# Kernel optimization log

Measured on AMD Instinct MI355X. Metric: run time of the kernel, lower is better.

The kernel has to match this reference:

```python
import jax, jax.numpy as jnp
import numpy as np

W_PAD = 1  # reflection pad / stencil half-width
CLAMP_MIN = 0.071
EPS = 1e-05


def _laplacian_kernel():
    k = 2 * W_PAD + 1
    ker = -jnp.ones((1, 1, k, k, k), dtype=jnp.float32)
    ker = ker.at[0, 0, W_PAD, W_PAD, W_PAD].set(float(k * k * k - 1))
    return ker  # [O=1, I=1, 3, 3, 3]


def _boundary_weight(pred):
    # pred: [B, L, D, H, W] raw logits
    B, L, D, H, Wd = pred.shape
    ps = jax.nn.softmax(pred, axis=1).astype(jnp.float32)
    # reflect-pad spatial dims by 1, then clamp (matches torch: pad then clamp)
    p = jnp.pad(ps, ((0, 0), (0, 0), (1, 1), (1, 1), (1, 1)), mode='reflect')
    p = jnp.clip(p, CLAMP_MIN)
    # single-channel 3x3x3 stencil applied independently per (batch, label)
    x = p.reshape(B * L, 1, D + 2, H + 2, Wd + 2)
    bt = jax.lax.conv_general_dilated(
        x, _laplacian_kernel(), window_strides=(1, 1, 1), padding='VALID',
        dimension_numbers=('NCDHW', 'OIDHW', 'NCDHW'))
    bt = jnp.abs(bt).reshape(B, L, D, H, Wd)
    bt = jax.lax.stop_gradient(bt)  # torch .detach()
    return 0.5 / (bt + 0.5)


def _dice_bpm(y_pred, y_true, bpm):
    vol_axes = tuple(range(2, y_pred.ndim))  # spatial dims
    top = 2.0 * jnp.sum(y_true * y_pred * bpm, axis=vol_axes)
    bottom = jnp.clip(jnp.sum((y_true + y_pred) * bpm, axis=vol_axes), EPS)
    return -jnp.mean(top / bottom)


def setup_inputs() -> dict:
    key = jax.random.key(0)
    k1, k2 = jax.random.split(key)
    shape = (2, 8, 128, 128, 128)
    pred = jax.random.normal(k1, shape, dtype=jnp.float32)
    target = jax.random.uniform(k2, shape, dtype=jnp.float32)
    return {"pred": pred, "target": target}


def reference(pred, target):
    focal_weight = _boundary_weight(pred)
    return _dice_bpm(pred, target, focal_weight)
```

## Files before the change

kernel.cpp:

```cpp
#include <hip/hip_runtime.h>
#include <hip/hip_fp16.h>

constexpr int Dd = 128, Hh = 128, Ww = 128;
constexpr int B_ = 2, L_ = 8;
constexpr int S_SP = Dd * Hh * Ww;
constexpr float CLAMP_MIN = 0.071f;
constexpr float EPS = 1e-5f;

constexpr int DCH = 8;
constexpr int NDC = Dd / DCH;
constexpr int NHG = Hh / 16;
constexpr int BLK_PER_P = NDC * NHG;
constexpr int NBLK2 = B_ * L_ * BLK_PER_P;

__global__ __launch_bounds__(256) void softmax_fp16_kernel(
    const float* __restrict__ pred, __half* __restrict__ ps) {
  const int S4 = S_SP / 4;
  int g = blockIdx.x * 256 + threadIdx.x;
  int b = g / S4;
  int s4 = g - b * S4;
  const float4* in = (const float4*)(pred + (size_t)b * L_ * S_SP) + s4;
  float v[L_][4];
#pragma unroll
  for (int l = 0; l < L_; ++l) {
    float4 t = in[(size_t)l * S4];
    v[l][0] = t.x; v[l][1] = t.y; v[l][2] = t.z; v[l][3] = t.w;
  }
#pragma unroll
  for (int c = 0; c < 4; ++c) {
    float m = v[0][c];
#pragma unroll
    for (int l = 1; l < L_; ++l) m = fmaxf(m, v[l][c]);
    float s = 0.f;
#pragma unroll
    for (int l = 0; l < L_; ++l) { v[l][c] = __expf(v[l][c] - m); s += v[l][c]; }
    float inv = 1.f / s;
#pragma unroll
    for (int l = 0; l < L_; ++l) v[l][c] = fmaxf(v[l][c] * inv, CLAMP_MIN);
  }
#pragma unroll
  for (int l = 0; l < L_; ++l) {
    __half2 h0 = __floats2half2_rn(v[l][0], v[l][1]);
    __half2 h1 = __floats2half2_rn(v[l][2], v[l][3]);
    uint2 u;
    u.x = *(unsigned*)&h0;
    u.y = *(unsigned*)&h1;
    *(uint2*)(ps + ((size_t)(b * L_ + l)) * S_SP + (size_t)s4 * 4) = u;
  }
}

__global__ __launch_bounds__(256) void stencil_dice_kernel(
    const __half* __restrict__ ps, const float* __restrict__ pred,
    const float* __restrict__ tgt, float* __restrict__ partial) {
  int blk = blockIdx.x;
  int dc = blk & 15;
  int hg = (blk >> 4) & 7;
  int bl = blk >> 7;
  int tid = threadIdx.x;
  int wl = tid & 15, hl = tid >> 4;
  int h = hg * 16 + hl;
  int w0 = wl * 8;
  int d0 = dc * DCH;
  const __half* P = ps + (size_t)bl * S_SP;
  int hm = (h == 0) ? 1 : h - 1;
  int hp = (h == Hh - 1) ? Hh - 2 : h + 1;
  int rows[3] = {hm, h, hp};

  float s2m[8], s2c[8], cprev[8];
  float top = 0.f, bot = 0.f;

  uint4  ubuf[2][3];
  float4 dbuf[2][4];

  auto loadPlane = [&](int t, uint4 u[3]) {
    int rt = t < 0 ? 1 : (t > Dd - 1 ? Dd - 2 : t);
    const __half* plane = P + (size_t)rt * Hh * Ww;
#pragma unroll
    for (int ri = 0; ri < 3; ++ri)
      u[ri] = *(const uint4*)(plane + rows[ri] * Ww + w0);
  };
  auto loadDice = [&](int d, float4 dv[4]) {
    size_t off = (size_t)bl * S_SP + (size_t)d * Hh * Ww + (size_t)h * Ww + w0;
    dv[0] = *(const float4*)(pred + off);
    dv[1] = *(const float4*)(pred + off + 4);
    dv[2] = *(const float4*)(tgt + off);
    dv[3] = *(const float4*)(tgt + off + 4);
  };

  loadPlane(d0 - 1, ubuf[0]);
  loadPlane(d0,     ubuf[1]);

#pragma unroll
  for (int k = 0; k < DCH + 2; ++k) {
    int t = d0 - 1 + k;
    float s2n[8], ctr[8];
#pragma unroll
    for (int w = 0; w < 8; ++w) s2n[w] = 0.f;
#pragma unroll
    for (int ri = 0; ri < 3; ++ri) {
      uint4 u = ubuf[k & 1][ri];
      float f[8];
      __half2 a;
      a = *(__half2*)&u.x; { float2 q = __half22float2(a); f[0] = q.x; f[1] = q.y; }
      a = *(__half2*)&u.y; { float2 q = __half22float2(a); f[2] = q.x; f[3] = q.y; }
      a = *(__half2*)&u.z; { float2 q = __half22float2(a); f[4] = q.x; f[5] = q.y; }
      a = *(__half2*)&u.w; { float2 q = __half22float2(a); f[6] = q.x; f[7] = q.y; }
      float lf = __shfl_up(f[7], 1, 64);
      if (wl == 0) lf = f[1];
      float rg = __shfl_down(f[0], 1, 64);
      if (wl == 15) rg = f[6];
      s2n[0] += lf + f[0] + f[1];
#pragma unroll
      for (int w = 1; w < 7; ++w) s2n[w] += f[w - 1] + f[w] + f[w + 1];
      s2n[7] += f[6] + f[7] + rg;
      if (ri == 1) {
#pragma unroll
        for (int w = 0; w < 8; ++w) ctr[w] = f[w];
      }
    }
    if (k >= 2) {
      const float4* dv = dbuf[(k + 1) & 1];
      float pv[8] = {dv[0].x, dv[0].y, dv[0].z, dv[0].w, dv[1].x, dv[1].y, dv[1].z, dv[1].w};
      float tv[8] = {dv[2].x, dv[2].y, dv[2].z, dv[2].w, dv[3].x, dv[3].y, dv[3].z, dv[3].w};
#pragma unroll
      for (int w = 0; w < 8; ++w) {
        float bt = fabsf(27.f * cprev[w] - (s2m[w] + s2c[w] + s2n[w]));
        float bw = 0.5f / (bt + 0.5f);
        top += tv[w] * pv[w] * bw;
        bot += (tv[w] + pv[w]) * bw;
      }
    }
#pragma unroll
    for (int w = 0; w < 8; ++w) { s2m[w] = s2c[w]; s2c[w] = s2n[w]; cprev[w] = ctr[w]; }
    if (k + 2 <= DCH + 1) loadPlane(t + 2, ubuf[k & 1]);
    if (k >= 1 && k <= DCH) loadDice(t, dbuf[k & 1]);
  }

#pragma unroll
  for (int o = 32; o > 0; o >>= 1) {
    top += __shfl_down(top, o, 64);
    bot += __shfl_down(bot, o, 64);
  }
  __shared__ float st[4], sb[4];
  int lane = tid & 63, wv = tid >> 6;
  if (lane == 0) { st[wv] = top; sb[wv] = bot; }
  __syncthreads();
  if (tid == 0) {
    partial[blk * 2 + 0] = st[0] + st[1] + st[2] + st[3];
    partial[blk * 2 + 1] = sb[0] + sb[1] + sb[2] + sb[3];
  }
}

__global__ void finalize_kernel(const float* __restrict__ partial, float* __restrict__ out) {
  __shared__ float rr[16];
  int t = threadIdx.x;
  int p = t >> 4, k = t & 15;
  float top = 0.f, bot = 0.f;
  for (int m = 0; m < BLK_PER_P / 16; ++m) {
    int blk = p * BLK_PER_P + k * (BLK_PER_P / 16) + m;
    top += partial[blk * 2 + 0];
    bot += partial[blk * 2 + 1];
  }
#pragma unroll
  for (int o = 8; o > 0; o >>= 1) {
    top += __shfl_down(top, o, 16);
    bot += __shfl_down(bot, o, 16);
  }
  if (k == 0) rr[p] = 2.f * top / fmaxf(bot, EPS);
  __syncthreads();
  if (t == 0) {
    float s = 0.f;
#pragma unroll
    for (int i = 0; i < 16; ++i) s += rr[i];
    out[0] = -s / 16.f;
  }
}

extern "C" void kernel_launch(void* const* d_in, const int* in_sizes, int n_in,
                              void* d_out, int out_size, void* d_ws, size_t ws_size,
                              hipStream_t stream) {
  const float* pred = (const float*)d_in[0];
  const float* tgt  = (const float*)d_in[1];
  __half* ps = (__half*)d_ws;
  float* partial = (float*)((char*)d_ws + (size_t)B_ * L_ * S_SP * sizeof(__half));

  int g1 = (B_ * (S_SP / 4)) / 256;
  softmax_fp16_kernel<<<g1, 256, 0, stream>>>(pred, ps);
  stencil_dice_kernel<<<NBLK2, 256, 0, stream>>>(ps, pred, tgt, partial);
  finalize_kernel<<<1, 256, 0, stream>>>(partial, (float*)d_out);
}
```

Before: 311.1 us.

## Fuse softmax into stencil-dice kernel, recomputing softmax per stencil row

```diff
diff --git a/kernel.cpp b/kernel.cpp
--- a/kernel.cpp
+++ b/kernel.cpp
@@ -1,165 +1,162 @@
 #include <hip/hip_runtime.h>
-#include <hip/hip_fp16.h>
 
 constexpr int Dd = 128, Hh = 128, Ww = 128;
 constexpr int B_ = 2, L_ = 8;
-constexpr int S_SP = Dd * Hh * Ww;
+constexpr int HW = Hh * Ww;
+constexpr int S_SP = Dd * HW;
 constexpr float CLAMP_MIN = 0.071f;
 constexpr float EPS = 1e-5f;
 
 constexpr int DCH = 8;
 constexpr int NDC = Dd / DCH;
-constexpr int NHG = Hh / 16;
-constexpr int BLK_PER_P = NDC * NHG;
-constexpr int NBLK2 = B_ * L_ * BLK_PER_P;
+constexpr int HT = 8;
+constexpr int NHG = Hh / HT;
+constexpr int NBLK = B_ * NDC * NHG;
 
-__global__ __launch_bounds__(256) void softmax_fp16_kernel(
-    const float* __restrict__ pred, __half* __restrict__ ps) {
-  const int S4 = S_SP / 4;
-  int g = blockIdx.x * 256 + threadIdx.x;
-  int b = g / S4;
-  int s4 = g - b * S4;
-  const float4* in = (const float4*)(pred + (size_t)b * L_ * S_SP) + s4;
-  float v[L_][4];
+__global__ __launch_bounds__(512) void fused_kernel(
+    const float* __restrict__ pred, const float* __restrict__ tgt,
+    float* __restrict__ partial) {
+  const int blk = blockIdx.x;
+  const int dc = blk & (NDC - 1);
+  const int hg = (blk >> 4) & (NHG - 1);
+  const int b  = blk >> 8;
+  const int tid = threadIdx.x;
+  const int wl = tid & 63;
+  const int hl = tid >> 6;
+  const int h = hg * HT + hl;
+  const int w0 = wl * 2;
+  const int d0 = dc * DCH;
+  const int hm = (h == 0) ? 1 : h - 1;
+  const int hp = (h == Hh - 1) ? Hh - 2 : h + 1;
+  const int rows[3] = {hm, h, hp};
+  const float* Pb = pred + (size_t)b * L_ * S_SP;
+  const float* Tb = tgt  + (size_t)b * L_ * S_SP;
+
+  float s2m[L_][2], s2c[L_][2], cprev[L_][2], rawprev[L_][2];
+  float top[L_], bot[L_];
 #pragma unroll
   for (int l = 0; l < L_; ++l) {
-    float4 t = in[(size_t)l * S4];
-    v[l][0] = t.x; v[l][1] = t.y; v[l][2] = t.z; v[l][3] = t.w;
+    top[l] = 0.f; bot[l] = 0.f;
+    s2m[l][0] = s2m[l][1] = 0.f;
+    s2c[l][0] = s2c[l][1] = 0.f;
+    cprev[l][0] = cprev[l][1] = 0.f;
+    rawprev[l][0] = rawprev[l][1] = 0.f;
   }
-#pragma unroll
-  for (int c = 0; c < 4; ++c) {
-    float m = v[0][c];
-#pragma unroll
-    for (int l = 1; l < L_; ++l) m = fmaxf(m, v[l][c]);
-    float s = 0.f;
-#pragma unroll
-    for (int l = 0; l < L_; ++l) { v[l][c] = __expf(v[l][c] - m); s += v[l][c]; }
-    float inv = 1.f / s;
-#pragma unroll
-    for (int l = 0; l < L_; ++l) v[l][c] = fmaxf(v[l][c] * inv, CLAMP_MIN);
-  }
-#pragma unroll
-  for (int l = 0; l < L_; ++l) {
-    __half2 h0 = __floats2half2_rn(v[l][0], v[l][1]);
-    __half2 h1 = __floats2half2_rn(v[l][2], v[l][3]);
-    uint2 u;
-    u.x = *(unsigned*)&h0;
-    u.y = *(unsigned*)&h1;
-    *(uint2*)(ps + ((size_t)(b * L_ + l)) * S_SP + (size_t)s4 * 4) = u;
-  }
-}
-
-__global__ __launch_bounds__(256) void stencil_dice_kernel(
-    const __half* __restrict__ ps, const float* __restrict__ pred,
-    const float* __restrict__ tgt, float* __restrict__ partial) {
-  int blk = blockIdx.x;
-  int dc = blk & 15;
-  int hg = (blk >> 4) & 7;
-  int bl = blk >> 7;
-  int tid = threadIdx.x;
-  int wl = tid & 15, hl = tid >> 4;
-  int h = hg * 16 + hl;
-  int w0 = wl * 8;
-  int d0 = dc * DCH;
-  const __half* P = ps + (size_t)bl * S_SP;
-  int hm = (h == 0) ? 1 : h - 1;
-  int hp = (h == Hh - 1) ? Hh - 2 : h + 1;
-  int rows[3] = {hm, h, hp};
-
-  float s2m[8], s2c[8], cprev[8];
-  float top = 0.f, bot = 0.f;
-
-  uint4  ubuf[2][3];
-  float4 dbuf[2][4];
-
-  auto loadPlane = [&](int t, uint4 u[3]) {
-    int rt = t < 0 ? 1 : (t > Dd - 1 ? Dd - 2 : t);
-    const __half* plane = P + (size_t)rt * Hh * Ww;
-#pragma unroll
-    for (int ri = 0; ri < 3; ++ri)
-      u[ri] = *(const uint4*)(plane + rows[ri] * Ww + w0);
-  };
-  auto loadDice = [&](int d, float4 dv[4]) {
-    size_t off = (size_t)bl * S_SP + (size_t)d * Hh * Ww + (size_t)h * Ww + w0;
-    dv[0] = *(const float4*)(pred + off);
-    dv[1] = *(const float4*)(pred + off + 4);
-    dv[2] = *(const float4*)(tgt + off);
-    dv[3] = *(const float4*)(tgt + off + 4);
-  };
-
-  loadPlane(d0 - 1, ubuf[0]);
-  loadPlane(d0,     ubuf[1]);
 
 #pragma unroll
   for (int k = 0; k < DCH + 2; ++k) {
-    int t = d0 - 1 + k;
-    float s2n[8], ctr[8];
+    const int t = d0 - 1 + k;
+    const int rt = (t < 0) ? 1 : ((t > Dd - 1) ? Dd - 2 : t);
+    float s2n[L_][2], ctr[L_][2], rawc[L_][2];
 #pragma unroll
-    for (int w = 0; w < 8; ++w) s2n[w] = 0.f;
+    for (int l = 0; l < L_; ++l) s2n[l][0] = s2n[l][1] = 0.f;
+
 #pragma unroll
     for (int ri = 0; ri < 3; ++ri) {
-      uint4 u = ubuf[k & 1][ri];
-      float f[8];
-      __half2 a;
-      a = *(__half2*)&u.x; { float2 q = __half22float2(a); f[0] = q.x; f[1] = q.y; }
-      a = *(__half2*)&u.y; { float2 q = __half22float2(a); f[2] = q.x; f[3] = q.y; }
-      a = *(__half2*)&u.z; { float2 q = __half22float2(a); f[4] = q.x; f[5] = q.y; }
-      a = *(__half2*)&u.w; { float2 q = __half22float2(a); f[6] = q.x; f[7] = q.y; }
-      float lf = __shfl_up(f[7], 1, 64);
-      if (wl == 0) lf = f[1];
-      float rg = __shfl_down(f[0], 1, 64);
-      if (wl == 15) rg = f[6];
-      s2n[0] += lf + f[0] + f[1];
+      const float* rp = Pb + (size_t)rt * HW + (size_t)rows[ri] * Ww + w0;
+      float2 v[L_];
 #pragma unroll
-      for (int w = 1; w < 7; ++w) s2n[w] += f[w - 1] + f[w] + f[w + 1];
-      s2n[7] += f[6] + f[7] + rg;
-      if (ri == 1) {
+      for (int l = 0; l < L_; ++l)
+        v[l] = *(const float2*)(rp + (size_t)l * S_SP);
+      float m0 = v[0].x, m1 = v[0].y;
 #pragma unroll
-        for (int w = 0; w < 8; ++w) ctr[w] = f[w];
+      for (int l = 1; l < L_; ++l) { m0 = fmaxf(m0, v[l].x); m1 = fmaxf(m1, v[l].y); }
+      float p0[L_], p1[L_];
+      float s0 = 0.f, s1 = 0.f;
+#pragma unroll
+      for (int l = 0; l < L_; ++l) {
+        p0[l] = __expf(v[l].x - m0); s0 += p0[l];
+        p1[l] = __expf(v[l].y - m1); s1 += p1[l];
+      }
+      const float i0 = 1.f / s0, i1 = 1.f / s1;
+#pragma unroll
+      for (int l = 0; l < L_; ++l) {
+        p0[l] = fmaxf(p0[l] * i0, CLAMP_MIN);
+        p1[l] = fmaxf(p1[l] * i1, CLAMP_MIN);
+      }
+#pragma unroll
+      for (int l = 0; l < L_; ++l) {
+        float lf = __shfl_up(p1[l], 1, 64);
+        if (wl == 0) lf = p1[l];
+        float rf = __shfl_down(p0[l], 1, 64);
+        if (wl == 63) rf = p0[l];
+        s2n[l][0] += lf + p0[l] + p1[l];
+        s2n[l][1] += p0[l] + p1[l] + rf;
+        if (ri == 1) {
+          ctr[l][0] = p0[l]; ctr[l][1] = p1[l];
+          rawc[l][0] = v[l].x; rawc[l][1] = v[l].y;
+        }
       }
     }
+
     if (k >= 2) {
-      const float4* dv = dbuf[(k + 1) & 1];
-      float pv[8] = {dv[0].x, dv[0].y, dv[0].z, dv[0].w, dv[1].x, dv[1].y, dv[1].z, dv[1].w};
-      float tv[8] = {dv[2].x, dv[2].y, dv[2].z, dv[2].w, dv[3].x, dv[3].y, dv[3].z, dv[3].w};
+      const int d = t - 1;
+      const size_t base = (size_t)d * HW + (size_t)h * Ww + w0;
 #pragma unroll
-      for (int w = 0; w < 8; ++w) {
-        float bt = fabsf(27.f * cprev[w] - (s2m[w] + s2c[w] + s2n[w]));
-        float bw = 0.5f / (bt + 0.5f);
-        top += tv[w] * pv[w] * bw;
-        bot += (tv[w] + pv[w]) * bw;
+      for (int l = 0; l < L_; ++l) {
+        const float2 tv = *(const float2*)(Tb + (size_t)l * S_SP + base);
+        {
+          float bt = fabsf(27.f * cprev[l][0] - (s2m[l][0] + s2c[l][0] + s2n[l][0]));
+          float bw = 0.5f / (bt + 0.5f);
+          top[l] += tv.x * rawprev[l][0] * bw;
+          bot[l] += (tv.x + rawprev[l][0]) * bw;
+        }
+        {
+          float bt = fabsf(27.f * cprev[l][1] - (s2m[l][1] + s2c[l][1] + s2n[l][1]));
+          float bw = 0.5f / (bt + 0.5f);
+          top[l] += tv.y * rawprev[l][1] * bw;
+          bot[l] += (tv.y + rawprev[l][1]) * bw;
+        }
       }
     }
+
 #pragma unroll
-    for (int w = 0; w < 8; ++w) { s2m[w] = s2c[w]; s2c[w] = s2n[w]; cprev[w] = ctr[w]; }
-    if (k + 2 <= DCH + 1) loadPlane(t + 2, ubuf[k & 1]);
-    if (k >= 1 && k <= DCH) loadDice(t, dbuf[k & 1]);
+    for (int l = 0; l < L_; ++l) {
+      s2m[l][0] = s2c[l][0]; s2m[l][1] = s2c[l][1];
+      s2c[l][0] = s2n[l][0]; s2c[l][1] = s2n[l][1];
+      cprev[l][0] = ctr[l][0]; cprev[l][1] = ctr[l][1];
+      rawprev[l][0] = rawc[l][0]; rawprev[l][1] = rawc[l][1];
+    }
   }
 
 #pragma unroll
-  for (int o = 32; o > 0; o >>= 1) {
-    top += __shfl_down(top, o, 64);
-    bot += __shfl_down(bot, o, 64);
+  for (int l = 0; l < L_; ++l) {
+#pragma unroll
+    for (int o = 32; o > 0; o >>= 1) {
+      top[l] += __shfl_down(top[l], o, 64);
+      bot[l] += __shfl_down(bot[l], o, 64);
+    }
   }
-  __shared__ float st[4], sb[4];
-  int lane = tid & 63, wv = tid >> 6;
-  if (lane == 0) { st[wv] = top; sb[wv] = bot; }
+  __shared__ float red[8][16];
+  const int wv = tid >> 6;
+  if (wl == 0) {
+#pragma unroll
+    for (int l = 0; l < L_; ++l) {
+      red[wv][2 * l]     = top[l];
+      red[wv][2 * l + 1] = bot[l];
+    }
+  }
   __syncthreads();
-  if (tid == 0) {
-    partial[blk * 2 + 0] = st[0] + st[1] + st[2] + st[3];
-    partial[blk * 2 + 1] = sb[0] + sb[1] + sb[2] + sb[3];
+  if (tid < 16) {
+    float s = 0.f;
+#pragma unroll
+    for (int w = 0; w < 8; ++w) s += red[w][tid];
+    partial[blk * 16 + tid] = s;
   }
 }
 
 __global__ void finalize_kernel(const float* __restrict__ partial, float* __restrict__ out) {
   __shared__ float rr[16];
-  int t = threadIdx.x;
-  int p = t >> 4, k = t & 15;
+  const int t = threadIdx.x;
+  const int p = t >> 4;
+  const int k = t & 15;
+  const int b = p >> 3;
+  const int l = p & 7;
   float top = 0.f, bot = 0.f;
-  for (int m = 0; m < BLK_PER_P / 16; ++m) {
-    int blk = p * BLK_PER_P + k * (BLK_PER_P / 16) + m;
-    top += partial[blk * 2 + 0];
-    bot += partial[blk * 2 + 1];
+  for (int m = 0; m < 16; ++m) {
+    int blk = b * (NDC * NHG) + k * 16 + m;
+    top += partial[blk * 16 + 2 * l];
+    bot += partial[blk * 16 + 2 * l + 1];
   }
 #pragma unroll
   for (int o = 8; o > 0; o >>= 1) {
@@ -181,11 +178,7 @@
                               hipStream_t stream) {
   const float* pred = (const float*)d_in[0];
   const float* tgt  = (const float*)d_in[1];
-  __half* ps = (__half*)d_ws;
-  float* partial = (float*)((char*)d_ws + (size_t)B_ * L_ * S_SP * sizeof(__half));
-
-  int g1 = (B_ * (S_SP / 4)) / 256;
-  softmax_fp16_kernel<<<g1, 256, 0, stream>>>(pred, ps);
-  stencil_dice_kernel<<<NBLK2, 256, 0, stream>>>(ps, pred, tgt, partial);
+  float* partial = (float*)d_ws;
+  fused_kernel<<<NBLK, 512, 0, stream>>>(pred, tgt, partial);
   finalize_kernel<<<1, 256, 0, stream>>>(partial, (float*)d_out);
 }
```

Measured after the change: 451.7 us. 45.2% more time.
